# Kernel optimization log

Measured on AMD Instinct MI355X. Metric: run time of the kernel, lower is better.

The kernel has to match this reference:

```python
import jax, jax.numpy as jnp
import numpy as np

HEAD_DIM = 256
N_Q = 8
N_KV = 4
HIDDEN = 2304
WINDOW = 1024
SOFT_CAP = 50.0
MAX_WAVELENGTH = 10000.0


def _rope(x, start_index=0):
    # x: [b, s, n, h]. keras_hub RotaryEmbedding (rotate-half convention),
    # followed by Gemma's interleave permutation of the feature dim.
    b, s, n, h = x.shape
    inv_freq = 1.0 / (MAX_WAVELENGTH ** (jnp.arange(0, h, 2, dtype=jnp.float32) / h))
    pos = jnp.arange(s, dtype=jnp.float32) + start_index
    freq = pos[:, None] * inv_freq[None, :]            # [s, h/2]
    emb = jnp.concatenate([freq, freq], axis=-1)[None, :, None, :]  # [1, s, 1, h]
    cos, sin = jnp.cos(emb).astype(x.dtype), jnp.sin(emb).astype(x.dtype)
    x1, x2 = jnp.split(x, 2, axis=-1)
    rot = jnp.concatenate([-x2, x1], axis=-1)
    y = x * cos + rot * sin
    # Gemma _apply_rope: split halves then interleave (same permutation on q and k)
    a, b2 = jnp.split(y, 2, axis=-1)
    return jnp.stack([a, b2], axis=-1).reshape(x.shape)


def setup_inputs() -> dict:
    key = jax.random.key(0)
    ks = jax.random.split(key, 5)
    B, T, D = 2, 2048, HIDDEN
    x = jax.random.normal(ks[0], (B, T, D), dtype=jnp.float32)
    # causal mask [b, q_len, kv_len]
    causal = jnp.tril(jnp.ones((T, T), dtype=bool))
    attention_mask = jnp.broadcast_to(causal[None], (B, T, T))
    scale = 0.02
    Wq = jax.random.normal(ks[1], (N_Q, D, HEAD_DIM), dtype=jnp.float32) * scale
    Wk = jax.random.normal(ks[2], (N_KV, D, HEAD_DIM), dtype=jnp.float32) * scale
    Wv = jax.random.normal(ks[3], (N_KV, D, HEAD_DIM), dtype=jnp.float32) * scale
    Wo = jax.random.normal(ks[4], (N_Q, HEAD_DIM, D), dtype=jnp.float32) * scale
    return {"x": x, "attention_mask": attention_mask, "Wq": Wq, "Wk": Wk, "Wv": Wv, "Wo": Wo}


def reference(x, attention_mask, Wq, Wk, Wv, Wo):
    b, t, d = x.shape
    q = jnp.einsum('btd,ndh->btnh', x, Wq)
    k = jnp.einsum('bsd,kdh->bskh', x, Wk)
    v = jnp.einsum('bsd,kdh->bskh', x, Wv)
    q = _rope(q)
    k = _rope(k)
    s = k.shape[1]
    # sliding window band mask (triu(-w+1) & tril(w-1)), rows sliced at cache_update_index=0
    i = jnp.arange(s)[:, None]
    j = jnp.arange(s)[None, :]
    sliding = (j - i <= WINDOW - 1) & (i - j <= WINDOW - 1)
    mask = attention_mask & sliding[None, :t, :s]      # [b, t, s]
    q = q * jnp.asarray(1.0 / np.sqrt(HEAD_DIM), dtype=q.dtype)
    g = N_Q // N_KV
    qg = q.reshape(b, t, N_KV, g, HEAD_DIM)
    logits = jnp.einsum('btkgh,bskh->bkgts', qg, k).astype(jnp.float32)
    logits = jnp.tanh(logits / SOFT_CAP) * SOFT_CAP    # logit soft-cap
    m = mask[:, None, None, :, :]                      # [b, 1, 1, t, s]
    logits = jnp.where(m, logits, jnp.float32(-1e30))
    probs = jax.nn.softmax(logits, axis=-1).astype(q.dtype)
    out = jnp.einsum('bkgts,bskh->btkgh', probs, v).reshape(b, t, N_Q, HEAD_DIM)
    no_attended = jnp.all(~attention_mask, axis=-1, keepdims=True)[..., None]  # [b, t, 1, 1]
    out = jnp.where(no_attended, jnp.zeros_like(out), out)
    return jnp.einsum('btnh,nhd->btd', out, Wo)
```

## Files before the change

kernel.cpp:

```cpp
#include <hip/hip_runtime.h>
#include <math.h>

#define HEAD_DIM 256
#define N_Q 8
#define N_KV 4
#define HIDDEN 2304
#define WINDOW 1024
#define BATCH 2
#define SEQ 2048
#define BT (BATCH*SEQ)

typedef unsigned short u16;
typedef __attribute__((ext_vector_type(8))) short bf16x8;
typedef __attribute__((ext_vector_type(4))) float f32x4;

__device__ __forceinline__ u16 f2bf(float f) {
    union { float f; unsigned u; } c; c.f = f;
    unsigned r = c.u + 0x7FFF + ((c.u >> 16) & 1);
    return (u16)(r >> 16);
}
__device__ __forceinline__ float bf2f(u16 b) {
    union { float f; unsigned u; } c; c.u = ((unsigned)b) << 16;
    return c.f;
}

__global__ __launch_bounds__(256) void prep_kernel(
    const float* __restrict__ x,
    const float* __restrict__ Wq, const float* __restrict__ Wk,
    const float* __restrict__ Wv, const float* __restrict__ Wo,
    u16* __restrict__ xb, u16* __restrict__ wt1, u16* __restrict__ wot)
{
    __shared__ float t[64][65];
    const int bx  = blockIdx.x;
    const int tid = threadIdx.x;

    if (bx < 4608) {
        const int i = bx * 256 + tid;
        const float4 a = ((const float4*)x)[2*i];
        const float4 b = ((const float4*)x)[2*i+1];
        u16 o[8] = { f2bf(a.x), f2bf(a.y), f2bf(a.z), f2bf(a.w),
                     f2bf(b.x), f2bf(b.y), f2bf(b.z), f2bf(b.w) };
        ((uint4*)xb)[i] = *(const uint4*)o;
        return;
    }

    if (bx < 6912) {
        const int b   = bx - 4608;
        const int j   = b / 144;
        const int rem = b % 144;
        const int d0  = (rem % 36) * 64;
        const int h0  = (rem / 36) * 64;
        const float* W = (j < 8)  ? Wq + (size_t)j*HIDDEN*HEAD_DIM
                       : (j < 12) ? Wk + (size_t)(j-8)*HIDDEN*HEAD_DIM
                                  : Wv + (size_t)(j-12)*HIDDEN*HEAD_DIM;
        {
            const int r = tid >> 4, c4 = tid & 15;
            #pragma unroll
            for (int rr = r; rr < 64; rr += 16) {
                const float4 v = *(const float4*)(W + (size_t)(d0+rr)*HEAD_DIM + h0 + c4*4);
                t[rr][c4*4+0] = v.x; t[rr][c4*4+1] = v.y;
                t[rr][c4*4+2] = v.z; t[rr][c4*4+3] = v.w;
            }
        }
        __syncthreads();
        {
            const int hh = tid >> 2;
            #pragma unroll
            for (int it = 0; it < 2; it++) {
                const int chunk = (tid & 3) + it*4;
                u16 tmp[8];
                #pragma unroll
                for (int jj = 0; jj < 8; jj++) tmp[jj] = f2bf(t[chunk*8+jj][hh]);
                *(uint4*)&wt1[(size_t)(j*256 + h0 + hh)*HIDDEN + d0 + chunk*8] = *(const uint4*)tmp;
            }
        }
        return;
    }

    {
        const int b  = bx - 6912;
        const int k0 = (b & 31) * 64;
        const int d0 = (b >> 5) * 64;
        {
            const int r = tid >> 4, c4 = tid & 15;
            #pragma unroll
            for (int rr = r; rr < 64; rr += 16) {
                const float4 v = *(const float4*)(Wo + (size_t)(k0+rr)*HIDDEN + d0 + c4*4);
                t[rr][c4*4+0] = v.x; t[rr][c4*4+1] = v.y;
                t[rr][c4*4+2] = v.z; t[rr][c4*4+3] = v.w;
            }
        }
        __syncthreads();
        {
            const int dd = tid >> 2;
            #pragma unroll
            for (int it = 0; it < 2; it++) {
                const int chunk = (tid & 3) + it*4;
                u16 tmp[8];
                #pragma unroll
                for (int jj = 0; jj < 8; jj++) tmp[jj] = f2bf(t[chunk*8+jj][dd]);
                *(uint4*)&wot[(size_t)(d0 + dd)*(N_Q*HEAD_DIM) + k0 + chunk*8] = *(const uint4*)tmp;
            }
        }
    }
}

template<int KK>
__device__ __forceinline__ void g256_ld_b(const u16 (&BsB)[16384], bf16x8 (&bf)[4],
                                          int wcol, int l16, int quad, int axor)
{
    #pragma unroll
    for (int j = 0; j < 4; j++)
        bf[j] = *(const bf16x8*)(&BsB[(wcol*64 + j*16 + l16)*64 + (((KK<<2)|quad)^axor)*8]);
}
template<int MH, int KK>
__device__ __forceinline__ void g256_ld_a(const u16 (&AsB)[16384], bf16x8 (&af)[4],
                                          int wrow, int l16, int quad, int axor)
{
    #pragma unroll
    for (int i = 0; i < 4; i++)
        af[i] = *(const bf16x8*)(&AsB[(wrow*128 + MH*64 + i*16 + l16)*64 + (((KK<<2)|quad)^axor)*8]);
}
template<int MH>
__device__ __forceinline__ void g256_mfma(const bf16x8 (&af)[4], const bf16x8 (&bf)[4],
                                          f32x4 (&acc)[8][4])
{
    __builtin_amdgcn_s_setprio(1);
    #pragma unroll
    for (int i = 0; i < 4; i++)
        #pragma unroll
        for (int j = 0; j < 4; j++)
            acc[MH*4+i][j] = __builtin_amdgcn_mfma_f32_16x16x32_bf16(
                                 af[i], bf[j], acc[MH*4+i][j], 0, 0, 0);
    __builtin_amdgcn_s_setprio(0);
}

#define STG256(DST, SRCP, R0, KT)                                              \
    __builtin_amdgcn_global_load_lds(                                          \
        (const __attribute__((address_space(1))) unsigned int*)                \
            ((SRCP) + (size_t)(R0)*K + (size_t)(KT)*64),                       \
        (__attribute__((address_space(3))) unsigned int*)                      \
            (&DST[((R0) + wave*8)*64]),                                        \
        16, 0, 0)

#define WAITV(N) asm volatile("s_waitcnt vmcnt(" #N ")" ::: "memory")
#define BAR()    __builtin_amdgcn_s_barrier()

template<typename OutT>
__global__ __launch_bounds__(512, 2) void gemm256_kernel(
    const u16* __restrict__ A, const u16* __restrict__ Bt,
    OutT* __restrict__ C, int M, int N, int K)
{
    __shared__ __align__(16) u16 As0[16384];
    __shared__ __align__(16) u16 As1[16384];
    __shared__ __align__(16) u16 Bs0[16384];
    __shared__ __align__(16) u16 Bs1[16384];

    const int nwg = gridDim.x;
    const int bid = blockIdx.x;
    const int cpx = nwg >> 3;
    const int swz = (bid & 7) * cpx + (bid >> 3);
    const int NX  = N >> 8;
    const int m0  = (swz / NX) << 8;
    const int n0  = (swz % NX) << 8;

    const int tid  = threadIdx.x;
    const int lane = tid & 63;
    const int wave = tid >> 6;
    const int wrow = wave >> 2;
    const int wcol = wave & 3;
    const int l16  = lane & 15;
    const int quad = lane >> 4;
    const int axor = l16 & 7;

    const int srow8  = lane >> 3;
    const int schunk = (lane & 7) ^ srow8;
    const u16* Ag = A  + (size_t)(m0 + wave*8 + srow8)*K + schunk*8;
    const u16* Bg = Bt + (size_t)(n0 + wave*8 + srow8)*K + schunk*8;

    f32x4 acc[8][4];
    #pragma unroll
    for (int i = 0; i < 8; i++)
        #pragma unroll
        for (int j = 0; j < 4; j++) acc[i][j] = (f32x4){0.f,0.f,0.f,0.f};
    bf16x8 af[4], bf[4];

    STG256(Bs0, Bg,   0, 0); STG256(Bs0, Bg,  64, 0);
    STG256(Bs0, Bg, 128, 0); STG256(Bs0, Bg, 192, 0);
    STG256(As0, Ag,   0, 0); STG256(As0, Ag, 128, 0);
    STG256(As0, Ag,  64, 0); STG256(As0, Ag, 192, 0);
    STG256(Bs1, Bg,   0, 1); STG256(Bs1, Bg,  64, 1);
    WAITV(4);
    BAR();

    const int NT2 = K >> 7;
    for (int t = 0; t < NT2; ++t) {
        const int T1 = 2*t+1, T2 = 2*t+2, T3 = 2*t+3;
        const bool nl = (t < NT2-1);

        g256_ld_b<0>(Bs0, bf, wcol, l16, quad, axor);
        g256_ld_a<0,0>(As0, af, wrow, l16, quad, axor);
        STG256(Bs1, Bg, 128, T1); STG256(Bs1, Bg, 192, T1);
        BAR();
        g256_mfma<0>(af, bf, acc);
        WAITV(4);
        BAR();

        g256_ld_a<1,0>(As0, af, wrow, l16, quad, axor);
        STG256(As1, Ag, 0, T1); STG256(As1, Ag, 128, T1);
        BAR();
        g256_mfma<1>(af, bf, acc);
        BAR();

        g256_ld_b<1>(Bs0, bf, wcol, l16, quad, axor);
        g256_ld_a<0,1>(As0, af, wrow, l16, quad, axor);
        STG256(As1, Ag, 64, T1); STG256(As1, Ag, 192, T1);
        BAR();
        g256_mfma<0>(af, bf, acc);
        BAR();

        g256_ld_a<1,1>(As0, af, wrow, l16, quad, axor);
        if (nl) { STG256(Bs0, Bg, 0, T2); STG256(Bs0, Bg, 64, T2); }
        BAR();
        g256_mfma<1>(af, bf, acc);
        if (nl) { WAITV(4); }
        else    { WAITV(0); }
        BAR();

        g256_ld_b<0>(Bs1, bf, wcol, l16, quad, axor);
        g256_ld_a<0,0>(As1, af, wrow, l16, quad, axor);
        if (nl) { STG256(Bs0, Bg, 128, T2); STG256(Bs0, Bg, 192, T2); }
        BAR();
        g256_mfma<0>(af, bf, acc);
        WAITV(4);
        BAR();

        g256_ld_a<1,0>(As1, af, wrow, l16, quad, axor);
        if (nl) { STG256(As0, Ag, 0, T2); STG256(As0, Ag, 128, T2); }
        BAR();
        g256_mfma<1>(af, bf, acc);
        BAR();

        g256_ld_b<1>(Bs1, bf, wcol, l16, quad, axor);
        g256_ld_a<0,1>(As1, af, wrow, l16, quad, axor);
        if (nl) { STG256(As0, Ag, 64, T2); STG256(As0, Ag, 192, T2); }
        BAR();
        g256_mfma<0>(af, bf, acc);
        BAR();

        g256_ld_a<1,1>(As1, af, wrow, l16, quad, axor);
        if (nl) { STG256(Bs1, Bg, 0, T3); STG256(Bs1, Bg, 64, T3); }
        BAR();
        g256_mfma<1>(af, bf, acc);
        WAITV(4);
        BAR();
    }

    #pragma unroll
    for (int ii = 0; ii < 8; ii++) {
        const int rbase = m0 + wrow*128 + ii*16 + quad*4;
        #pragma unroll
        for (int j = 0; j < 4; j++) {
            const int col = n0 + wcol*64 + j*16 + l16;
            #pragma unroll
            for (int r = 0; r < 4; r++) {
                const float v = acc[ii][j][r];
                if constexpr (sizeof(OutT) == 2)
                    ((u16*)C)[(size_t)(rbase + r)*N + col] = f2bf(v);
                else
                    ((float*)C)[(size_t)(rbase + r)*N + col] = v;
            }
        }
    }
}

#undef STG256

__global__ __launch_bounds__(256) void ropevt_kernel(
    const u16* __restrict__ raw, u16* __restrict__ qb,
    u16* __restrict__ kbf, u16* __restrict__ vtt)
{
    __shared__ u16 T[32*264];
    const int bx  = blockIdx.x;
    const int tid = threadIdx.x;

    if (bx < BT) {
        const int r   = bx;
        const int pos = r & (SEQ-1);
        const u16* row = raw + (size_t)r * 4096;
        const float LOG1E4 = 9.210340371976184f;

        #pragma unroll
        for (int p = tid; p < 1024; p += 256) {
            const int n = p >> 7, j = p & 127;
            const float lo = bf2f(row[n*256 + j]);
            const float hi = bf2f(row[n*256 + j + 128]);
            const float inv = __expf(-LOG1E4 * (float)j * (1.0f/128.0f));
            float s, c; sincosf((float)pos * inv, &s, &c);
            qb[((size_t)r*N_Q + n)*HEAD_DIM + j]       = f2bf((lo*c - hi*s) * 0.0625f);
            qb[((size_t)r*N_Q + n)*HEAD_DIM + j + 128] = f2bf((hi*c + lo*s) * 0.0625f);
        }
        #pragma unroll
        for (int p = tid; p < 512; p += 256) {
            const int n = p >> 7, j = p & 127;
            const float lo = bf2f(row[2048 + n*256 + j]);
            const float hi = bf2f(row[2048 + n*256 + j + 128]);
            const float inv = __expf(-LOG1E4 * (float)j * (1.0f/128.0f));
            float s, c; sincosf((float)pos * inv, &s, &c);
            kbf[((size_t)r*N_KV + n)*HEAD_DIM + j]       = f2bf(lo*c - hi*s);
            kbf[((size_t)r*N_KV + n)*HEAD_DIM + j + 128] = f2bf(hi*c + lo*s);
        }
        return;
    }

    {
        const int blk = bx - BT;
        const int sc  = blk & 63;
        const int bk  = blk >> 6;
        const int b   = bk >> 2, kh = bk & 3;

        const u16* rrow = raw + (size_t)(b*SEQ + sc*32)*4096 + 3072 + kh*256;
        {
            const int s = tid >> 3;
            #pragma unroll
            for (int it = 0; it < 4; it++) {
                const int seg = (tid & 7) + it*8;
                *(uint4*)&T[s*264 + seg*8] = *(const uint4*)(rrow + (size_t)s*4096 + seg*8);
            }
        }
        __syncthreads();
        u16* out = vtt + (size_t)blk*8192;
        #pragma unroll
        for (int it = 0; it < 4; it++) {
            const int o = tid + it*256;
            const int h = o >> 2, ss = o & 3;
            u16 tmp[8];
            #pragma unroll
            for (int j = 0; j < 8; j++) tmp[j] = T[(ss*8 + j)*264 + h];
            *(uint4*)(out + h*32 + ((ss ^ (h & 3))*8)) = *(const uint4*)tmp;
        }
    }
}

#define AQT 64
__global__ __launch_bounds__(256) void attn_mfma_kernel(
    const u16* __restrict__ qb, const u16* __restrict__ kb,
    const u16* __restrict__ vtt, u16* __restrict__ ao)
{
    __shared__ u16 Ks[32*264];
    __shared__ u16 Vs[256*32];
    __shared__ u16 Ps[64*40];
    __shared__ float lsum[64];

    const int qh = blockIdx.y;
    const int kh = qh >> 1;
    const int bx = ((blockIdx.y >> 2) & 1) ? (gridDim.x - 1 - (int)blockIdx.x)
                                           : (int)blockIdx.x;
    const int t0 = bx * AQT;
    const int b  = t0 >> 11;
    const int tb = t0 & (SEQ-1);
    const int tid  = threadIdx.x;
    const int wave = tid >> 6;
    const int lane = tid & 63;
    const int l16  = lane & 15;
    const int quad = lane >> 4;

    bf16x8 qf[8];
    {
        const u16* qrow = qb + ((size_t)(t0 + wave*16 + l16)*N_Q + qh)*HEAD_DIM + quad*8;
        #pragma unroll
        for (int c = 0; c < 8; c++) qf[c] = *(const bf16x8*)(qrow + c*32);
    }

    f32x4 o[4][4];
    #pragma unroll
    for (int i = 0; i < 4; i++)
        #pragma unroll
        for (int j = 0; j < 4; j++) o[i][j] = (f32x4){0.f,0.f,0.f,0.f};
    float lpart[4] = {0.f, 0.f, 0.f, 0.f};

    int s_begin = tb - (WINDOW-1); if (s_begin < 0) s_begin = 0;
    const int st0 = s_begin & ~31;

    const u16* kbase = kb  + ((size_t)(b*SEQ)*N_KV + kh)*HEAD_DIM;
    const u16* vbase = vtt + ((size_t)(b*N_KV + kh)*SEQ)*HEAD_DIM;

    for (int st = st0; st < tb + AQT; st += 32) {
        __syncthreads();
        {
            const u16* vtile = vbase + (size_t)st*HEAD_DIM;
            #pragma unroll
            for (int c = 0; c < 4; c++) {
                const int off = wave*2048 + c*512;
                __builtin_amdgcn_global_load_lds(
                    (const __attribute__((address_space(1))) unsigned int*)(vtile + off + lane*8),
                    (__attribute__((address_space(3))) unsigned int*)&Vs[off],
                    16, 0, 0);
            }
            const int s = tid >> 3;
            const u16* krow = kbase + (size_t)(st + s)*(N_KV*HEAD_DIM);
            #pragma unroll
            for (int it = 0; it < 4; it++) {
                const int seg = (tid & 7) + it*8;
                *(uint4*)&Ks[s*264 + seg*8] = *(const uint4*)(krow + seg*8);
            }
        }
        __syncthreads();

        f32x4 sc[2];
        #pragma unroll
        for (int sf = 0; sf < 2; sf++) {
            f32x4 a = (f32x4){0.f,0.f,0.f,0.f};
            const u16* kr = &Ks[(sf*16 + l16)*264 + quad*8];
            #pragma unroll
            for (int c = 0; c < 8; c++)
                a = __builtin_amdgcn_mfma_f32_16x16x32_bf16(
                        qf[c], *(const bf16x8*)(kr + c*32), a, 0, 0, 0);
            sc[sf] = a;
        }

        #pragma unroll
        for (int sf = 0; sf < 2; sf++) {
            const int sg = st + sf*16 + l16;
            #pragma unroll
            for (int r = 0; r < 4; r++) {
                const int tg = tb + wave*16 + quad*4 + r;
                const float e1 = __expf(sc[sf][r] * 0.04f);
                float p = __expf(-100.0f / (e1 + 1.0f));
                const bool ok = (sg <= tg) && (tg - sg < WINDOW);
                p = ok ? p : 0.0f;
                lpart[r] += p;
                Ps[(wave*16 + quad*4 + r)*40 + sf*16 + l16] = f2bf(p);
            }
        }
        __syncthreads();

        bf16x8 ap[4];
        #pragma unroll
        for (int i = 0; i < 4; i++)
            ap[i] = *(const bf16x8*)&Ps[(i*16 + l16)*40 + quad*8];
        #pragma unroll
        for (int j = 0; j < 4; j++) {
            const int hr = wave*64 + j*16 + l16;
            const bf16x8 bv = *(const bf16x8*)&Vs[hr*32 + ((quad ^ (l16 & 3))*8)];
            #pragma unroll
            for (int i = 0; i < 4; i++)
                o[i][j] = __builtin_amdgcn_mfma_f32_16x16x32_bf16(ap[i], bv, o[i][j], 0, 0, 0);
        }
    }

    #pragma unroll
    for (int r = 0; r < 4; r++) {
        float s = lpart[r];
        #pragma unroll
        for (int sh = 1; sh <= 8; sh <<= 1) s += __shfl_xor(s, sh, 64);
        if (l16 == 0) lsum[wave*16 + quad*4 + r] = s;
    }
    __syncthreads();

    #pragma unroll
    for (int i = 0; i < 4; i++) {
        #pragma unroll
        for (int r = 0; r < 4; r++) {
            const int rl  = i*16 + quad*4 + r;
            const float inv = 1.0f / (lsum[rl] + 1e-30f);
            u16* arow = ao + ((size_t)(t0 + rl)*N_Q + qh)*HEAD_DIM + wave*64 + l16;
            #pragma unroll
            for (int j = 0; j < 4; j++)
                arow[j*16] = f2bf(o[i][j][r] * inv);
        }
    }
}

extern "C" void kernel_launch(void* const* d_in, const int* in_sizes, int n_in,
                              void* d_out, int out_size, void* d_ws, size_t ws_size,
                              hipStream_t stream)
{
    const float* x  = (const float*)d_in[0];
    const float* Wq = (const float*)d_in[2];
    const float* Wk = (const float*)d_in[3];
    const float* Wv = (const float*)d_in[4];
    const float* Wo = (const float*)d_in[5];
    float* out = (float*)d_out;

    char* w = (char*)d_ws;
    u16* qbuf = (u16*)(w);
    u16* kbuf = (u16*)(w +  16777216ull);
    u16* vtt  = (u16*)(w +  25165824ull);
    u16* aob  = (u16*)(w +  33554432ull);
    u16* xb   = (u16*)(w +  50331648ull);
    u16* wt1  = (u16*)(w +  69206016ull);
    u16* wot  = (u16*)(w +  88080384ull);
    u16* raw  = (u16*)(w +  97517568ull);

    prep_kernel<<<8064, 256, 0, stream>>>(x, Wq, Wk, Wv, Wo, xb, wt1, wot);

    gemm256_kernel<u16><<<(BT/256)*(4096/256), 512, 0, stream>>>(
        xb, wt1, raw, BT, 4096, HIDDEN);

    ropevt_kernel<<<BT + BATCH*N_KV*64, 256, 0, stream>>>(raw, qbuf, kbuf, vtt);

    attn_mfma_kernel<<<dim3(BT/AQT, N_Q), 256, 0, stream>>>(qbuf, kbuf, vtt, aob);

    gemm256_kernel<float><<<(BT/256)*(HIDDEN/256), 512, 0, stream>>>(
        aob, wot, out, BT, HIDDEN, N_Q*HEAD_DIM);
}
```

Measured before the change: 367.3 us.

## Shrink GEMM tiles to 256x128 with 4 waves and 32-wide K steps

Replaces the 256x256-tile, 512-thread GEMM with a 256x128-tile, 256-thread kernel that stages K in 32-element slices. It uses a new XOR swizzle and a simpler double-buffered loop that fully drains outstanding loads every half-iteration. The aim is to double the block count, especially for the output projection, which previously launched fewer blocks than there are CUs, and to cut LDS per block. The cost is less data reuse per tile, more barriers and waits per unit of K, and weaker overlap of loads with MFMA work.

```diff
diff --git a/kernel.cpp b/kernel.cpp
--- a/kernel.cpp
+++ b/kernel.cpp
@@ -105,24 +105,25 @@
     }
 }
 
-template<int KK>
-__device__ __forceinline__ void g256_ld_b(const u16 (&BsB)[16384], bf16x8 (&bf)[4],
-                                          int wcol, int l16, int quad, int axor)
-{
+__device__ __forceinline__ void g128_ld_b(const u16 (&Bs)[4096], bf16x8 (&bf)[4],
+                                          int wcol, int l16, int quad)
+{
+    const int slot = quad ^ ((l16 >> 1) & 3);
     #pragma unroll
     for (int j = 0; j < 4; j++)
-        bf[j] = *(const bf16x8*)(&BsB[(wcol*64 + j*16 + l16)*64 + (((KK<<2)|quad)^axor)*8]);
-}
-template<int MH, int KK>
-__device__ __forceinline__ void g256_ld_a(const u16 (&AsB)[16384], bf16x8 (&af)[4],
-                                          int wrow, int l16, int quad, int axor)
-{
+        bf[j] = *(const bf16x8*)(&Bs[(wcol*64 + j*16 + l16)*32 + slot*8]);
+}
+template<int MH>
+__device__ __forceinline__ void g128_ld_a(const u16 (&As)[8192], bf16x8 (&af)[4],
+                                          int wrow, int l16, int quad)
+{
+    const int slot = quad ^ ((l16 >> 1) & 3);
     #pragma unroll
     for (int i = 0; i < 4; i++)
-        af[i] = *(const bf16x8*)(&AsB[(wrow*128 + MH*64 + i*16 + l16)*64 + (((KK<<2)|quad)^axor)*8]);
+        af[i] = *(const bf16x8*)(&As[(wrow*128 + MH*64 + i*16 + l16)*32 + slot*8]);
 }
 template<int MH>
-__device__ __forceinline__ void g256_mfma(const bf16x8 (&af)[4], const bf16x8 (&bf)[4],
+__device__ __forceinline__ void g128_mfma(const bf16x8 (&af)[4], const bf16x8 (&bf)[4],
                                           f32x4 (&acc)[8][4])
 {
     __builtin_amdgcn_s_setprio(1);
@@ -135,48 +136,47 @@
     __builtin_amdgcn_s_setprio(0);
 }
 
-#define STG256(DST, SRCP, R0, KT)                                              \
+#define STG128(DST, SRCP, R0, KT)                                              \
     __builtin_amdgcn_global_load_lds(                                          \
         (const __attribute__((address_space(1))) unsigned int*)                \
-            ((SRCP) + (size_t)(R0)*K + (size_t)(KT)*64),                       \
+            ((SRCP) + (size_t)(R0)*K + (size_t)(KT)*32),                       \
         (__attribute__((address_space(3))) unsigned int*)                      \
-            (&DST[((R0) + wave*8)*64]),                                        \
+            (&DST[((R0) + wave*16)*32]),                                       \
         16, 0, 0)
 
 #define WAITV(N) asm volatile("s_waitcnt vmcnt(" #N ")" ::: "memory")
 #define BAR()    __builtin_amdgcn_s_barrier()
 
 template<typename OutT>
-__global__ __launch_bounds__(512, 2) void gemm256_kernel(
+__global__ __launch_bounds__(256, 2) void gemm128_kernel(
     const u16* __restrict__ A, const u16* __restrict__ Bt,
     OutT* __restrict__ C, int M, int N, int K)
 {
-    __shared__ __align__(16) u16 As0[16384];
-    __shared__ __align__(16) u16 As1[16384];
-    __shared__ __align__(16) u16 Bs0[16384];
-    __shared__ __align__(16) u16 Bs1[16384];
+    __shared__ __align__(16) u16 As0[8192];
+    __shared__ __align__(16) u16 As1[8192];
+    __shared__ __align__(16) u16 Bs0[4096];
+    __shared__ __align__(16) u16 Bs1[4096];
 
     const int nwg = gridDim.x;
     const int bid = blockIdx.x;
     const int cpx = nwg >> 3;
     const int swz = (bid & 7) * cpx + (bid >> 3);
-    const int NX  = N >> 8;
+    const int NX  = N >> 7;
     const int m0  = (swz / NX) << 8;
-    const int n0  = (swz % NX) << 8;
+    const int n0  = (swz % NX) << 7;
 
     const int tid  = threadIdx.x;
     const int lane = tid & 63;
     const int wave = tid >> 6;
-    const int wrow = wave >> 2;
-    const int wcol = wave & 3;
+    const int wrow = wave >> 1;
+    const int wcol = wave & 1;
     const int l16  = lane & 15;
     const int quad = lane >> 4;
-    const int axor = l16 & 7;
-
-    const int srow8  = lane >> 3;
-    const int schunk = (lane & 7) ^ srow8;
-    const u16* Ag = A  + (size_t)(m0 + wave*8 + srow8)*K + schunk*8;
-    const u16* Bg = Bt + (size_t)(n0 + wave*8 + srow8)*K + schunk*8;
+
+    const int srow   = lane >> 2;
+    const int schunk = (lane & 3) ^ ((lane >> 3) & 3);
+    const u16* Ag = A  + (size_t)(m0 + wave*16 + srow)*K + schunk*8;
+    const u16* Bg = Bt + (size_t)(n0 + wave*16 + srow)*K + schunk*8;
 
     f32x4 acc[8][4];
     #pragma unroll
@@ -185,74 +185,48 @@
         for (int j = 0; j < 4; j++) acc[i][j] = (f32x4){0.f,0.f,0.f,0.f};
     bf16x8 af[4], bf[4];
 
-    STG256(Bs0, Bg,   0, 0); STG256(Bs0, Bg,  64, 0);
-    STG256(Bs0, Bg, 128, 0); STG256(Bs0, Bg, 192, 0);
-    STG256(As0, Ag,   0, 0); STG256(As0, Ag, 128, 0);
-    STG256(As0, Ag,  64, 0); STG256(As0, Ag, 192, 0);
-    STG256(Bs1, Bg,   0, 1); STG256(Bs1, Bg,  64, 1);
-    WAITV(4);
+    const int NT = K >> 5;
+
+    STG128(As0, Ag,   0, 0); STG128(As0, Ag,  64, 0);
+    STG128(As0, Ag, 128, 0); STG128(As0, Ag, 192, 0);
+    STG128(Bs0, Bg,   0, 0); STG128(Bs0, Bg,  64, 0);
+    WAITV(0);
     BAR();
 
-    const int NT2 = K >> 7;
-    for (int t = 0; t < NT2; ++t) {
-        const int T1 = 2*t+1, T2 = 2*t+2, T3 = 2*t+3;
-        const bool nl = (t < NT2-1);
-
-        g256_ld_b<0>(Bs0, bf, wcol, l16, quad, axor);
-        g256_ld_a<0,0>(As0, af, wrow, l16, quad, axor);
-        STG256(Bs1, Bg, 128, T1); STG256(Bs1, Bg, 192, T1);
-        BAR();
-        g256_mfma<0>(af, bf, acc);
-        WAITV(4);
-        BAR();
-
-        g256_ld_a<1,0>(As0, af, wrow, l16, quad, axor);
-        STG256(As1, Ag, 0, T1); STG256(As1, Ag, 128, T1);
-        BAR();
-        g256_mfma<1>(af, bf, acc);
-        BAR();
-
-        g256_ld_b<1>(Bs0, bf, wcol, l16, quad, axor);
-        g256_ld_a<0,1>(As0, af, wrow, l16, quad, axor);
-        STG256(As1, Ag, 64, T1); STG256(As1, Ag, 192, T1);
-        BAR();
-        g256_mfma<0>(af, bf, acc);
-        BAR();
-
-        g256_ld_a<1,1>(As0, af, wrow, l16, quad, axor);
-        if (nl) { STG256(Bs0, Bg, 0, T2); STG256(Bs0, Bg, 64, T2); }
-        BAR();
-        g256_mfma<1>(af, bf, acc);
-        if (nl) { WAITV(4); }
-        else    { WAITV(0); }
-        BAR();
-
-        g256_ld_b<0>(Bs1, bf, wcol, l16, quad, axor);
-        g256_ld_a<0,0>(As1, af, wrow, l16, quad, axor);
-        if (nl) { STG256(Bs0, Bg, 128, T2); STG256(Bs0, Bg, 192, T2); }
-        BAR();
-        g256_mfma<0>(af, bf, acc);
-        WAITV(4);
-        BAR();
-
-        g256_ld_a<1,0>(As1, af, wrow, l16, quad, axor);
-        if (nl) { STG256(As0, Ag, 0, T2); STG256(As0, Ag, 128, T2); }
-        BAR();
-        g256_mfma<1>(af, bf, acc);
-        BAR();
-
-        g256_ld_b<1>(Bs1, bf, wcol, l16, quad, axor);
-        g256_ld_a<0,1>(As1, af, wrow, l16, quad, axor);
-        if (nl) { STG256(As0, Ag, 64, T2); STG256(As0, Ag, 192, T2); }
-        BAR();
-        g256_mfma<0>(af, bf, acc);
-        BAR();
-
-        g256_ld_a<1,1>(As1, af, wrow, l16, quad, axor);
-        if (nl) { STG256(Bs1, Bg, 0, T3); STG256(Bs1, Bg, 64, T3); }
-        BAR();
-        g256_mfma<1>(af, bf, acc);
-        WAITV(4);
+    const int NI = NT >> 1;
+    for (int t = 0; t < NI; ++t) {
+        const int T1 = 2*t+1, T2 = 2*t+2;
+        const bool nl = (t < NI-1);
+
+        g128_ld_b(Bs0, bf, wcol, l16, quad);
+        g128_ld_a<0>(As0, af, wrow, l16, quad);
+        STG128(Bs1, Bg, 0, T1); STG128(Bs1, Bg, 64, T1);
+        STG128(As1, Ag, 0, T1);
+        BAR();
+        g128_mfma<0>(af, bf, acc);
+        BAR();
+
+        g128_ld_a<1>(As0, af, wrow, l16, quad);
+        STG128(As1, Ag, 64, T1); STG128(As1, Ag, 128, T1); STG128(As1, Ag, 192, T1);
+        BAR();
+        g128_mfma<1>(af, bf, acc);
+        WAITV(0);
+        BAR();
+
+        g128_ld_b(Bs1, bf, wcol, l16, quad);
+        g128_ld_a<0>(As1, af, wrow, l16, quad);
+        if (nl) { STG128(Bs0, Bg, 0, T2); STG128(Bs0, Bg, 64, T2);
+                  STG128(As0, Ag, 0, T2); }
+        BAR();
+        g128_mfma<0>(af, bf, acc);
+        BAR();
+
+        g128_ld_a<1>(As1, af, wrow, l16, quad);
+        if (nl) { STG128(As0, Ag, 64, T2); STG128(As0, Ag, 128, T2);
+                  STG128(As0, Ag, 192, T2); }
+        BAR();
+        g128_mfma<1>(af, bf, acc);
+        WAITV(0);
         BAR();
     }
 
@@ -274,7 +248,7 @@
     }
 }
 
-#undef STG256
+#undef STG128
 
 __global__ __launch_bounds__(256) void ropevt_kernel(
     const u16* __restrict__ raw, u16* __restrict__ qb,
@@ -495,13 +469,13 @@
 
     prep_kernel<<<8064, 256, 0, stream>>>(x, Wq, Wk, Wv, Wo, xb, wt1, wot);
 
-    gemm256_kernel<u16><<<(BT/256)*(4096/256), 512, 0, stream>>>(
+    gemm128_kernel<u16><<<(BT/256)*(4096/128), 256, 0, stream>>>(
         xb, wt1, raw, BT, 4096, HIDDEN);
 
     ropevt_kernel<<<BT + BATCH*N_KV*64, 256, 0, stream>>>(raw, qbuf, kbuf, vtt);
 
     attn_mfma_kernel<<<dim3(BT/AQT, N_Q), 256, 0, stream>>>(qbuf, kbuf, vtt, aob);
 
-    gemm256_kernel<float><<<(BT/256)*(HIDDEN/256), 512, 0, stream>>>(
+    gemm128_kernel<float><<<(BT/256)*(HIDDEN/128), 256, 0, stream>>>(
         aob, wot, out, BT, HIDDEN, N_Q*HEAD_DIM);
 }
```

Measured after the change: 376.6 us. 1.03x slower.

## Restructure gemm256 main loop into 4 phases with full-tile prefetch

Applied to the files above, without the earlier changes.

Rewrites the 256x256 GEMM K-loop from eight half-M phases into four full-M phases. Each wave now loads all eight A fragments at once and issues 32 MFMAs per phase. The global-to-LDS staging is reorganized so whole tiles are prefetched one tile ahead, with fewer barriers and waitcnts per K step. The aim is to cut barrier and sync overhead and raise MFMA density per phase. The cost is higher VGPR pressure from the larger A fragment array, which could hurt occupancy under launch_bounds(512,2), and the waitcnt/barrier ordering becomes harder to keep race-free.

```diff
diff --git a/kernel.cpp b/kernel.cpp
--- a/kernel.cpp
+++ b/kernel.cpp
@@ -113,25 +113,24 @@
     for (int j = 0; j < 4; j++)
         bf[j] = *(const bf16x8*)(&BsB[(wcol*64 + j*16 + l16)*64 + (((KK<<2)|quad)^axor)*8]);
 }
-template<int MH, int KK>
-__device__ __forceinline__ void g256_ld_a(const u16 (&AsB)[16384], bf16x8 (&af)[4],
-                                          int wrow, int l16, int quad, int axor)
-{
-    #pragma unroll
-    for (int i = 0; i < 4; i++)
-        af[i] = *(const bf16x8*)(&AsB[(wrow*128 + MH*64 + i*16 + l16)*64 + (((KK<<2)|quad)^axor)*8]);
-}
-template<int MH>
-__device__ __forceinline__ void g256_mfma(const bf16x8 (&af)[4], const bf16x8 (&bf)[4],
-                                          f32x4 (&acc)[8][4])
+template<int KK>
+__device__ __forceinline__ void g256_ld_a8(const u16 (&AsB)[16384], bf16x8 (&af)[8],
+                                           int wrow, int l16, int quad, int axor)
+{
+    #pragma unroll
+    for (int i = 0; i < 8; i++)
+        af[i] = *(const bf16x8*)(&AsB[(wrow*128 + i*16 + l16)*64 + (((KK<<2)|quad)^axor)*8]);
+}
+__device__ __forceinline__ void g256_mfma32(const bf16x8 (&af)[8], const bf16x8 (&bf)[4],
+                                            f32x4 (&acc)[8][4])
 {
     __builtin_amdgcn_s_setprio(1);
     #pragma unroll
-    for (int i = 0; i < 4; i++)
+    for (int i = 0; i < 8; i++)
         #pragma unroll
         for (int j = 0; j < 4; j++)
-            acc[MH*4+i][j] = __builtin_amdgcn_mfma_f32_16x16x32_bf16(
-                                 af[i], bf[j], acc[MH*4+i][j], 0, 0, 0);
+            acc[i][j] = __builtin_amdgcn_mfma_f32_16x16x32_bf16(
+                            af[i], bf[j], acc[i][j], 0, 0, 0);
     __builtin_amdgcn_s_setprio(0);
 }
 
@@ -183,76 +182,57 @@
     for (int i = 0; i < 8; i++)
         #pragma unroll
         for (int j = 0; j < 4; j++) acc[i][j] = (f32x4){0.f,0.f,0.f,0.f};
-    bf16x8 af[4], bf[4];
+    bf16x8 af[8], bf[4];
 
     STG256(Bs0, Bg,   0, 0); STG256(Bs0, Bg,  64, 0);
     STG256(Bs0, Bg, 128, 0); STG256(Bs0, Bg, 192, 0);
-    STG256(As0, Ag,   0, 0); STG256(As0, Ag, 128, 0);
-    STG256(As0, Ag,  64, 0); STG256(As0, Ag, 192, 0);
+    STG256(As0, Ag,   0, 0); STG256(As0, Ag,  64, 0);
+    STG256(As0, Ag, 128, 0); STG256(As0, Ag, 192, 0);
     STG256(Bs1, Bg,   0, 1); STG256(Bs1, Bg,  64, 1);
-    WAITV(4);
+    STG256(Bs1, Bg, 128, 1); STG256(Bs1, Bg, 192, 1);
+    STG256(As1, Ag,   0, 1); STG256(As1, Ag,  64, 1);
+    STG256(As1, Ag, 128, 1); STG256(As1, Ag, 192, 1);
+    WAITV(8);
     BAR();
 
     const int NT2 = K >> 7;
     for (int t = 0; t < NT2; ++t) {
-        const int T1 = 2*t+1, T2 = 2*t+2, T3 = 2*t+3;
+        const int T2 = 2*t+2, T3 = 2*t+3;
         const bool nl = (t < NT2-1);
 
         g256_ld_b<0>(Bs0, bf, wcol, l16, quad, axor);
-        g256_ld_a<0,0>(As0, af, wrow, l16, quad, axor);
-        STG256(Bs1, Bg, 128, T1); STG256(Bs1, Bg, 192, T1);
-        BAR();
-        g256_mfma<0>(af, bf, acc);
-        WAITV(4);
-        BAR();
-
-        g256_ld_a<1,0>(As0, af, wrow, l16, quad, axor);
-        STG256(As1, Ag, 0, T1); STG256(As1, Ag, 128, T1);
-        BAR();
-        g256_mfma<1>(af, bf, acc);
+        g256_ld_a8<0>(As0, af, wrow, l16, quad, axor);
+        BAR();
+        g256_mfma32(af, bf, acc);
         BAR();
 
         g256_ld_b<1>(Bs0, bf, wcol, l16, quad, axor);
-        g256_ld_a<0,1>(As0, af, wrow, l16, quad, axor);
-        STG256(As1, Ag, 64, T1); STG256(As1, Ag, 192, T1);
-        BAR();
-        g256_mfma<0>(af, bf, acc);
-        BAR();
-
-        g256_ld_a<1,1>(As0, af, wrow, l16, quad, axor);
-        if (nl) { STG256(Bs0, Bg, 0, T2); STG256(Bs0, Bg, 64, T2); }
-        BAR();
-        g256_mfma<1>(af, bf, acc);
+        g256_ld_a8<1>(As0, af, wrow, l16, quad, axor);
+        BAR();
+        if (nl) { STG256(Bs0, Bg, 0, T2); STG256(Bs0, Bg, 64, T2);
+                  STG256(Bs0, Bg, 128, T2); STG256(Bs0, Bg, 192, T2); }
+        g256_mfma32(af, bf, acc);
         if (nl) { WAITV(4); }
         else    { WAITV(0); }
         BAR();
 
         g256_ld_b<0>(Bs1, bf, wcol, l16, quad, axor);
-        g256_ld_a<0,0>(As1, af, wrow, l16, quad, axor);
-        if (nl) { STG256(Bs0, Bg, 128, T2); STG256(Bs0, Bg, 192, T2); }
-        BAR();
-        g256_mfma<0>(af, bf, acc);
-        WAITV(4);
-        BAR();
-
-        g256_ld_a<1,0>(As1, af, wrow, l16, quad, axor);
-        if (nl) { STG256(As0, Ag, 0, T2); STG256(As0, Ag, 128, T2); }
-        BAR();
-        g256_mfma<1>(af, bf, acc);
+        g256_ld_a8<0>(As1, af, wrow, l16, quad, axor);
+        if (nl) { STG256(As0, Ag, 0, T2); STG256(As0, Ag, 64, T2);
+                  STG256(As0, Ag, 128, T2); STG256(As0, Ag, 192, T2); }
+        BAR();
+        g256_mfma32(af, bf, acc);
         BAR();
 
         g256_ld_b<1>(Bs1, bf, wcol, l16, quad, axor);
-        g256_ld_a<0,1>(As1, af, wrow, l16, quad, axor);
-        if (nl) { STG256(As0, Ag, 64, T2); STG256(As0, Ag, 192, T2); }
-        BAR();
-        g256_mfma<0>(af, bf, acc);
-        BAR();
-
-        g256_ld_a<1,1>(As1, af, wrow, l16, quad, axor);
-        if (nl) { STG256(Bs1, Bg, 0, T3); STG256(Bs1, Bg, 64, T3); }
-        BAR();
-        g256_mfma<1>(af, bf, acc);
-        WAITV(4);
+        g256_ld_a8<1>(As1, af, wrow, l16, quad, axor);
+        BAR();
+        if (nl) { STG256(Bs1, Bg, 0, T3); STG256(Bs1, Bg, 64, T3);
+                  STG256(Bs1, Bg, 128, T3); STG256(Bs1, Bg, 192, T3);
+                  STG256(As1, Ag, 0, T3); STG256(As1, Ag, 64, T3);
+                  STG256(As1, Ag, 128, T3); STG256(As1, Ag, 192, T3); }
+        g256_mfma32(af, bf, acc);
+        if (nl) { WAITV(8); }
         BAR();
     }
 
```

Measured after the change: 399.1 us. +8.7%, slower.

## Double-buffer K/V/P tiles in LDS and prefetch next tile during compute

Applied to the files above, without the earlier changes.

The attention loop now ping-pongs between two sets of K, V and P shared-memory buffers. While the current tile runs its QK^T, soft-cap/exp and PV MFMAs, the next tile's V is issued with global_load_lds and its K is loaded into registers. The K registers are written to LDS after the softmax step. This hides global-load latency and cuts a barrier per step. In exchange, LDS use roughly doubles (about 76KB per block), which can lower the number of resident blocks per CU.

```diff
diff --git a/kernel.cpp b/kernel.cpp
--- a/kernel.cpp
+++ b/kernel.cpp
@@ -343,13 +343,83 @@
 }
 
 #define AQT 64
+
+#define ATTN_STEP(KSc, VSc, PSc, KSn, VSn, ST, NX)                              \
+{                                                                               \
+    uint4 kreg[4];                                                              \
+    if (NX) {                                                                   \
+        const u16* vtile = vbase + (size_t)((ST)+32)*HEAD_DIM;                  \
+        _Pragma("unroll")                                                       \
+        for (int c4 = 0; c4 < 4; c4++) {                                        \
+            const int off = wave*2048 + c4*512;                                 \
+            __builtin_amdgcn_global_load_lds(                                   \
+                (const __attribute__((address_space(1))) unsigned int*)(vtile + off + lane*8), \
+                (__attribute__((address_space(3))) unsigned int*)&VSn[off],     \
+                16, 0, 0);                                                      \
+        }                                                                       \
+        const u16* krow = kbase + (size_t)((ST)+32 + ks)*(N_KV*HEAD_DIM);       \
+        _Pragma("unroll")                                                       \
+        for (int it = 0; it < 4; it++)                                          \
+            kreg[it] = *(const uint4*)(krow + ((tid & 7) + it*8)*8);            \
+    }                                                                           \
+    f32x4 sc[2];                                                                \
+    _Pragma("unroll")                                                           \
+    for (int sf = 0; sf < 2; sf++) {                                            \
+        f32x4 a = (f32x4){0.f,0.f,0.f,0.f};                                     \
+        const u16* kr = &KSc[(sf*16 + l16)*264 + quad*8];                       \
+        _Pragma("unroll")                                                       \
+        for (int cc = 0; cc < 8; cc++)                                          \
+            a = __builtin_amdgcn_mfma_f32_16x16x32_bf16(                        \
+                    qf[cc], *(const bf16x8*)(kr + cc*32), a, 0, 0, 0);          \
+        sc[sf] = a;                                                             \
+    }                                                                           \
+    _Pragma("unroll")                                                           \
+    for (int sf = 0; sf < 2; sf++) {                                            \
+        const int sg = (ST) + sf*16 + l16;                                      \
+        _Pragma("unroll")                                                       \
+        for (int r = 0; r < 4; r++) {                                           \
+            const int tg = tb + wave*16 + quad*4 + r;                           \
+            const float e1 = __expf(sc[sf][r] * 0.04f);                         \
+            float p = __expf(-100.0f / (e1 + 1.0f));                            \
+            const bool ok = (sg <= tg) && (tg - sg < WINDOW);                   \
+            p = ok ? p : 0.0f;                                                  \
+            lpart[r] += p;                                                      \
+            PSc[(wave*16 + quad*4 + r)*40 + sf*16 + l16] = f2bf(p);             \
+        }                                                                       \
+    }                                                                           \
+    if (NX) {                                                                   \
+        _Pragma("unroll")                                                       \
+        for (int it = 0; it < 4; it++)                                          \
+            *(uint4*)&KSn[ks*264 + ((tid & 7) + it*8)*8] = kreg[it];            \
+    }                                                                           \
+    asm volatile("s_waitcnt lgkmcnt(0)" ::: "memory");                          \
+    __builtin_amdgcn_s_barrier();                                               \
+    bf16x8 ap[4];                                                               \
+    _Pragma("unroll")                                                           \
+    for (int i = 0; i < 4; i++)                                                 \
+        ap[i] = *(const bf16x8*)&PSc[(i*16 + l16)*40 + quad*8];                 \
+    _Pragma("unroll")                                                           \
+    for (int j = 0; j < 4; j++) {                                               \
+        const int hr = wave*64 + j*16 + l16;                                    \
+        const bf16x8 bv = *(const bf16x8*)&VSc[hr*32 + ((quad ^ (l16 & 3))*8)]; \
+        _Pragma("unroll")                                                       \
+        for (int i = 0; i < 4; i++)                                             \
+            o[i][j] = __builtin_amdgcn_mfma_f32_16x16x32_bf16(ap[i], bv, o[i][j], 0, 0, 0); \
+    }                                                                           \
+    if (NX) { asm volatile("s_waitcnt vmcnt(0)" ::: "memory"); }                \
+    __builtin_amdgcn_s_barrier();                                               \
+}
+
 __global__ __launch_bounds__(256) void attn_mfma_kernel(
     const u16* __restrict__ qb, const u16* __restrict__ kb,
     const u16* __restrict__ vtt, u16* __restrict__ ao)
 {
-    __shared__ u16 Ks[32*264];
-    __shared__ u16 Vs[256*32];
-    __shared__ u16 Ps[64*40];
+    __shared__ u16 Ks0[32*264];
+    __shared__ u16 Ks1[32*264];
+    __shared__ u16 Vs0[256*32];
+    __shared__ u16 Vs1[256*32];
+    __shared__ u16 Ps0[64*40];
+    __shared__ u16 Ps1[64*40];
     __shared__ float lsum[64];
 
     const int qh = blockIdx.y;
@@ -364,6 +434,7 @@
     const int lane = tid & 63;
     const int l16  = lane & 15;
     const int quad = lane >> 4;
+    const int ks   = tid >> 3;
 
     bf16x8 qf[8];
     {
@@ -385,68 +456,29 @@
     const u16* kbase = kb  + ((size_t)(b*SEQ)*N_KV + kh)*HEAD_DIM;
     const u16* vbase = vtt + ((size_t)(b*N_KV + kh)*SEQ)*HEAD_DIM;
 
-    for (int st = st0; st < tb + AQT; st += 32) {
-        __syncthreads();
-        {
-            const u16* vtile = vbase + (size_t)st*HEAD_DIM;
-            #pragma unroll
-            for (int c = 0; c < 4; c++) {
-                const int off = wave*2048 + c*512;
-                __builtin_amdgcn_global_load_lds(
-                    (const __attribute__((address_space(1))) unsigned int*)(vtile + off + lane*8),
-                    (__attribute__((address_space(3))) unsigned int*)&Vs[off],
-                    16, 0, 0);
-            }
-            const int s = tid >> 3;
-            const u16* krow = kbase + (size_t)(st + s)*(N_KV*HEAD_DIM);
-            #pragma unroll
-            for (int it = 0; it < 4; it++) {
-                const int seg = (tid & 7) + it*8;
-                *(uint4*)&Ks[s*264 + seg*8] = *(const uint4*)(krow + seg*8);
-            }
-        }
-        __syncthreads();
-
-        f32x4 sc[2];
-        #pragma unroll
-        for (int sf = 0; sf < 2; sf++) {
-            f32x4 a = (f32x4){0.f,0.f,0.f,0.f};
-            const u16* kr = &Ks[(sf*16 + l16)*264 + quad*8];
-            #pragma unroll
-            for (int c = 0; c < 8; c++)
-                a = __builtin_amdgcn_mfma_f32_16x16x32_bf16(
-                        qf[c], *(const bf16x8*)(kr + c*32), a, 0, 0, 0);
-            sc[sf] = a;
-        }
-
-        #pragma unroll
-        for (int sf = 0; sf < 2; sf++) {
-            const int sg = st + sf*16 + l16;
-            #pragma unroll
-            for (int r = 0; r < 4; r++) {
-                const int tg = tb + wave*16 + quad*4 + r;
-                const float e1 = __expf(sc[sf][r] * 0.04f);
-                float p = __expf(-100.0f / (e1 + 1.0f));
-                const bool ok = (sg <= tg) && (tg - sg < WINDOW);
-                p = ok ? p : 0.0f;
-                lpart[r] += p;
-                Ps[(wave*16 + quad*4 + r)*40 + sf*16 + l16] = f2bf(p);
-            }
-        }
-        __syncthreads();
-
-        bf16x8 ap[4];
-        #pragma unroll
-        for (int i = 0; i < 4; i++)
-            ap[i] = *(const bf16x8*)&Ps[(i*16 + l16)*40 + quad*8];
-        #pragma unroll
-        for (int j = 0; j < 4; j++) {
-            const int hr = wave*64 + j*16 + l16;
-            const bf16x8 bv = *(const bf16x8*)&Vs[hr*32 + ((quad ^ (l16 & 3))*8)];
-            #pragma unroll
-            for (int i = 0; i < 4; i++)
-                o[i][j] = __builtin_amdgcn_mfma_f32_16x16x32_bf16(ap[i], bv, o[i][j], 0, 0, 0);
-        }
+    {
+        const u16* vtile = vbase + (size_t)st0*HEAD_DIM;
+        #pragma unroll
+        for (int c4 = 0; c4 < 4; c4++) {
+            const int off = wave*2048 + c4*512;
+            __builtin_amdgcn_global_load_lds(
+                (const __attribute__((address_space(1))) unsigned int*)(vtile + off + lane*8),
+                (__attribute__((address_space(3))) unsigned int*)&Vs0[off],
+                16, 0, 0);
+        }
+        const u16* krow = kbase + (size_t)(st0 + ks)*(N_KV*HEAD_DIM);
+        #pragma unroll
+        for (int it = 0; it < 4; it++) {
+            const int seg = (tid & 7) + it*8;
+            *(uint4*)&Ks0[ks*264 + seg*8] = *(const uint4*)(krow + seg*8);
+        }
+    }
+    __syncthreads();
+
+    for (int st = st0; st < tb + AQT; st += 64) {
+        ATTN_STEP(Ks0, Vs0, Ps0, Ks1, Vs1, st, true);
+        const bool nx2 = (st + 64 < tb + AQT);
+        ATTN_STEP(Ks1, Vs1, Ps1, Ks0, Vs0, st + 32, nx2);
     }
 
     #pragma unroll
```

Result: slower. 383.4 us (+4.4%).
